# Performance work log

Measured on AMD Instinct MI355X. Metric: run time of the kernel, lower is better.

Reference implementation:

```python
import jax, jax.numpy as jnp
import numpy as np

N_ENT = 1000000
N_REL = 500
DIM = 128
BATCH = 16384


def setup_inputs() -> dict:
    key = jax.random.key(0)
    k1, k2, k3, k4, k5 = jax.random.split(key, 5)
    # sample[:,0]=head entity, [:,1]=relation, [:,2]=tail entity
    heads = jax.random.randint(k1, (BATCH, 1), 0, N_ENT)
    rels = jax.random.randint(k2, (BATCH, 1), 0, N_REL)
    tails = jax.random.randint(k3, (BATCH, 1), 0, N_ENT)
    sample = jnp.concatenate([heads, rels, tails], axis=1).astype(jnp.int64)
    # Xavier-uniform init: bound = sqrt(6/(fan_in+fan_out))
    b_e = float(np.sqrt(6.0 / (N_ENT + DIM)))
    b_r = float(np.sqrt(6.0 / (N_REL + DIM * DIM)))
    entity_embedding = jax.random.uniform(k4, (N_ENT, DIM), jnp.float32, -b_e, b_e)
    relation_embedding = jax.random.uniform(k5, (N_REL, DIM * DIM), jnp.float32, -b_r, b_r)
    return {"sample": sample, "entity_embedding": entity_embedding,
            "relation_embedding": relation_embedding}


def _l2norm(x, axis):
    # matches F.normalize(p=2): x / max(||x||, eps)
    n = jnp.sqrt(jnp.sum(x * x, axis=axis, keepdims=True))
    return x / jnp.maximum(n, 1e-12)


def reference(sample, entity_embedding, relation_embedding):
    h, r, t = sample[:, 0], sample[:, 1], sample[:, 2]
    A = _l2norm(entity_embedding[h], axis=-1)                 # [B, d]
    R = relation_embedding[r].reshape(-1, DIM, DIM)           # [B, d, d]
    A_T = _l2norm(entity_embedding[t], axis=-1)               # [B, d]
    tr = jnp.einsum('bij,bj->bi', R, A_T)                     # [B, d]
    return -jnp.sum(A * tr, axis=-1)                          # [B]
```

## Files before the change

kernel.cpp:

```cpp
#include <hip/hip_runtime.h>
#include <hip/hip_bf16.h>

#define DIM 128
#define BATCH 16384

__global__ __launch_bounds__(256)
void rescal_kernel(const int* __restrict__ sample,
                   const float* __restrict__ ent,
                   const float* __restrict__ rel,
                   float* __restrict__ out) {
    const int b   = blockIdx.x;
    const int tid = threadIdx.x;
    const int wave = tid >> 6;
    const int lane = tid & 63;

    const int h = sample[b * 3 + 0];
    const int r = sample[b * 3 + 1];
    const int t = sample[b * 3 + 2];

    __shared__ float sA[DIM];
    __shared__ float sT[DIM];
    __shared__ float red[4];

    float v;
    if (tid < DIM) v = ent[(size_t)h * DIM + tid];
    else           v = ent[(size_t)t * DIM + (tid - DIM)];

    float sq = v * v;
    #pragma unroll
    for (int o = 32; o > 0; o >>= 1) sq += __shfl_down(sq, o);
    if (lane == 0) red[wave] = sq;
    __syncthreads();

    const float sumA = red[0] + red[1];
    const float sumT = red[2] + red[3];
    const float inv = (tid < DIM) ? 1.0f / fmaxf(sqrtf(sumA), 1e-12f)
                                  : 1.0f / fmaxf(sqrtf(sumT), 1e-12f);
    if (tid < DIM) sA[tid] = v * inv;
    else           sT[tid - DIM] = v * inv;
    __syncthreads();

    const float4* __restrict__ R4 = (const float4*)(rel + (size_t)r * (DIM * DIM));
    const int j0 = (tid * 4) & (DIM - 1);
    const float t0 = sT[j0 + 0];
    const float t1 = sT[j0 + 1];
    const float t2 = sT[j0 + 2];
    const float t3 = sT[j0 + 3];
    const int row0 = tid >> 5;

    float acc = 0.0f;
    #pragma unroll
    for (int k = 0; k < 16; ++k) {
        const float4 rv = R4[k * 256 + tid];
        const float a = sA[k * 8 + row0];
        acc += a * (rv.x * t0 + rv.y * t1 + rv.z * t2 + rv.w * t3);
    }

    #pragma unroll
    for (int o = 32; o > 0; o >>= 1) acc += __shfl_down(acc, o);
    __syncthreads();
    if (lane == 0) red[wave] = acc;
    __syncthreads();
    if (tid == 0) out[b] = -(red[0] + red[1] + red[2] + red[3]);
}

extern "C" void kernel_launch(void* const* d_in, const int* in_sizes, int n_in,
                              void* d_out, int out_size, void* d_ws, size_t ws_size,
                              hipStream_t stream) {
    const int*   sample = (const int*)d_in[0];
    const float* ent    = (const float*)d_in[1];
    const float* rel    = (const float*)d_in[2];
    float*       out    = (float*)d_out;

    rescal_kernel<<<BATCH, 256, 0, stream>>>(sample, ent, rel, out);
}
```

Measured before the change: 684.5 us.

## Group samples by relation so each block loads its relation matrix once

Launches one block per relation instead of one per sample. Each block scans the whole sample array to collect the samples that use its relation, keeps the 128x128 relation matrix in registers, and scores those samples in chunks of 32, with head and tail embeddings staged in shared memory. This removes the repeated 64KB relation-matrix reads that each sample caused before. In exchange, every block scans all 16384 samples, only 500 blocks run, and relations with more than 2048 samples would silently drop the extra ones.

```diff
diff --git a/kernel.cpp b/kernel.cpp
--- a/kernel.cpp
+++ b/kernel.cpp
@@ -1,67 +1,107 @@
 #include <hip/hip_runtime.h>
-#include <hip/hip_bf16.h>
 
-#define DIM 128
+#define DIM   128
 #define BATCH 16384
+#define NREL  500
+#define CHUNK 32
+#define LCAP  2048
 
-__global__ __launch_bounds__(256)
-void rescal_kernel(const int* __restrict__ sample,
-                   const float* __restrict__ ent,
-                   const float* __restrict__ rel,
-                   float* __restrict__ out) {
-    const int b   = blockIdx.x;
-    const int tid = threadIdx.x;
+__global__ __launch_bounds__(256, 2)
+void score_k(const int* __restrict__ sample, const float* __restrict__ ent,
+             const float* __restrict__ rel, float* __restrict__ out) {
+    const int g    = blockIdx.x;
+    const int tid  = threadIdx.x;
+    const int lane = tid & 63;
     const int wave = tid >> 6;
-    const int lane = tid & 63;
+    const int row  = tid >> 1;
+    const int half = tid & 1;
 
-    const int h = sample[b * 3 + 0];
-    const int r = sample[b * 3 + 1];
-    const int t = sample[b * 3 + 2];
-
-    __shared__ float sA[DIM];
-    __shared__ float sT[DIM];
-    __shared__ float red[4];
-
-    float v;
-    if (tid < DIM) v = ent[(size_t)h * DIM + tid];
-    else           v = ent[(size_t)t * DIM + (tid - DIM)];
-
-    float sq = v * v;
-    #pragma unroll
-    for (int o = 32; o > 0; o >>= 1) sq += __shfl_down(sq, o);
-    if (lane == 0) red[wave] = sq;
+    __shared__ int sList[LCAP];
+    __shared__ int sCount;
+    if (tid == 0) sCount = 0;
     __syncthreads();
 
-    const float sumA = red[0] + red[1];
-    const float sumT = red[2] + red[3];
-    const float inv = (tid < DIM) ? 1.0f / fmaxf(sqrtf(sumA), 1e-12f)
-                                  : 1.0f / fmaxf(sqrtf(sumT), 1e-12f);
-    if (tid < DIM) sA[tid] = v * inv;
-    else           sT[tid - DIM] = v * inv;
+    for (int b = tid; b < BATCH; b += 256) {
+        if (sample[b * 3 + 1] == g) {
+            int p = atomicAdd(&sCount, 1);
+            if (p < LCAP) sList[p] = b;
+        }
+    }
     __syncthreads();
+    const int m = min(sCount, LCAP);
+    if (m == 0) return;
 
-    const float4* __restrict__ R4 = (const float4*)(rel + (size_t)r * (DIM * DIM));
-    const int j0 = (tid * 4) & (DIM - 1);
-    const float t0 = sT[j0 + 0];
-    const float t1 = sT[j0 + 1];
-    const float t2 = sT[j0 + 2];
-    const float t3 = sT[j0 + 3];
-    const int row0 = tid >> 5;
+    const float4* __restrict__ R4 = (const float4*)(rel + (size_t)g * (DIM * DIM));
+    float4 Rr[16];
+    #pragma unroll
+    for (int q = 0; q < 16; ++q)
+        Rr[q] = R4[row * 32 + half * 16 + q];
 
-    float acc = 0.0f;
-    #pragma unroll
-    for (int k = 0; k < 16; ++k) {
-        const float4 rv = R4[k * 256 + tid];
-        const float a = sA[k * 8 + row0];
-        acc += a * (rv.x * t0 + rv.y * t1 + rv.z * t2 + rv.w * t3);
+    __shared__ alignas(16) float sAT[CHUNK * 2 * DIM];
+    __shared__ float sNp[64][4];
+    __shared__ float sInv[64];
+    __shared__ float sRed[CHUNK * 4];
+
+    for (int base = 0; base < m; base += CHUNK) {
+        const int cact = min(CHUNK, m - base);
+
+        #pragma unroll
+        for (int p = 0; p < 8; ++p) {
+            int c = p * 4 + wave;
+            if (c < cact) {
+                int gi   = sList[base + c];
+                int eidx = (lane < 32) ? sample[gi * 3 + 0] : sample[gi * 3 + 2];
+                int e    = (lane & 31) * 4;
+                float4 v = *(const float4*)(ent + (size_t)eidx * DIM + e);
+                *(float4*)&sAT[c * 256 + (lane < 32 ? 0 : DIM) + e] = v;
+            }
+        }
+        __syncthreads();
+
+        {
+            int v = tid >> 2, q = tid & 3;
+            float s = 0.f;
+            if (v < cact * 2) {
+                const float4* p4 = (const float4*)&sAT[v * DIM + q * 32];
+                #pragma unroll
+                for (int j = 0; j < 8; ++j) {
+                    float4 x = p4[j];
+                    s += x.x * x.x + x.y * x.y + x.z * x.z + x.w * x.w;
+                }
+            }
+            sNp[v][q] = s;
+        }
+        __syncthreads();
+        if (tid < 64) {
+            float s = sNp[tid][0] + sNp[tid][1] + sNp[tid][2] + sNp[tid][3];
+            sInv[tid] = 1.0f / fmaxf(sqrtf(s), 1e-12f);
+        }
+
+        for (int c = 0; c < cact; ++c) {
+            const float4* T4 = (const float4*)&sAT[c * 256 + DIM + half * 64];
+            float acc = 0.f;
+            #pragma unroll
+            for (int q = 0; q < 16; ++q) {
+                float4 tv = T4[q];
+                acc = fmaf(Rr[q].x, tv.x, acc);
+                acc = fmaf(Rr[q].y, tv.y, acc);
+                acc = fmaf(Rr[q].z, tv.z, acc);
+                acc = fmaf(Rr[q].w, tv.w, acc);
+            }
+            float pt = sAT[c * 256 + row] * acc;
+            #pragma unroll
+            for (int o = 32; o > 0; o >>= 1) pt += __shfl_down(pt, o);
+            if (lane == 0) sRed[c * 4 + wave] = pt;
+        }
+        __syncthreads();
+
+        if (tid < cact) {
+            float s = sRed[tid * 4] + sRed[tid * 4 + 1]
+                    + sRed[tid * 4 + 2] + sRed[tid * 4 + 3];
+            out[sList[base + tid]] = -s * sInv[tid * 2] * sInv[tid * 2 + 1];
+        }
+        __syncthreads();
     }
-
-    #pragma unroll
-    for (int o = 32; o > 0; o >>= 1) acc += __shfl_down(acc, o);
-    __syncthreads();
-    if (lane == 0) red[wave] = acc;
-    __syncthreads();
-    if (tid == 0) out[b] = -(red[0] + red[1] + red[2] + red[3]);
 }
 
 extern "C" void kernel_launch(void* const* d_in, const int* in_sizes, int n_in,
@@ -72,5 +112,5 @@
     const float* rel    = (const float*)d_in[2];
     float*       out    = (float*)d_out;
 
-    rescal_kernel<<<BATCH, 256, 0, stream>>>(sample, ent, rel, out);
+    score_k<<<NREL, 256, 0, stream>>>(sample, ent, rel, out);
 }
```

Measured after the change: 629.8 us. 8.0% less time.
